# Performance work log

Measured on AMD Instinct MI355X. Metric: run time of the kernel, lower is better.

Reference implementation:

```python
import jax, jax.numpy as jnp
import numpy as np

B, CIN, H, W, OC = 32, 64, 32, 128, 128


def setup_inputs() -> dict:
    key = jax.random.key(0)
    ks = jax.random.split(key, 5)
    scale_x = (6.0 / (CIN + 5 * OC)) ** 0.5  # xavier-uniform-like std scale
    scale_h = (6.0 / (OC + 5 * OC)) ** 0.5
    return {
        "x": jax.random.normal(ks[0], (B, CIN, H, W), jnp.float32),
        "w0": jax.random.normal(ks[1], (4, CIN, 5 * OC), jnp.float32) * scale_x,
        "u0": jax.random.normal(ks[2], (4, OC, 5 * OC), jnp.float32) * scale_h,
        "u1": jax.random.normal(ks[3], (4, OC, 5 * OC), jnp.float32) * scale_h,
        "b": jax.random.uniform(ks[4], (4, 5 * OC), jnp.float32),
    }


def _flip(x, d):
    # direction 0: identity; 1: flip width; 2: flip height; 3: flip both
    if d == 1:
        return x[:, :, :, ::-1]
    if d == 2:
        return x[:, :, ::-1, :]
    if d == 3:
        return x[:, :, ::-1, ::-1]
    return x


def _scan_direction(x, w0, u0, u1, b):
    """2D LSTM raster-order recurrence via anti-diagonal wavefronts.
    x: (B, CIN, H, W) already flipped. Returns (B, OC, H, W) in the flipped frame
    (the original module folds hidden states without flipping back)."""
    Bb, Cin, Hh, Ww = x.shape
    oc = u0.shape[0]
    K = min(Hh, Ww)  # max wavefront length
    xh = jnp.transpose(x, (2, 3, 0, 1))              # (H, W, B, Cin)
    gx_all = jnp.einsum('hwbc,cg->hwbg', xh, w0) + b  # input projection (H,W,B,5oc)
    c0 = jnp.zeros((Hh, Ww, Bb, oc), x.dtype)
    h0 = jnp.zeros_like(c0)
    ks = jnp.arange(K)

    def step(carry, d):
        c_state, h_state = carry
        y0 = jnp.maximum(0, d - (Ww - 1))
        ys = y0 + ks
        xs = d - ys
        valid = (ys <= jnp.minimum(d, Hh - 1)) & (xs >= 0) & (xs < Ww)
        ysc = jnp.clip(ys, 0, Hh - 1)
        xsc = jnp.clip(xs, 0, Ww - 1)
        gx = gx_all[ysc, xsc]  # (K, B, 5oc)
        m_up = ((ys > 0) & valid)[:, None, None]
        m_lf = ((xs > 0) & valid)[:, None, None]
        yu = jnp.clip(ys - 1, 0, Hh - 1)
        xl = jnp.clip(xs - 1, 0, Ww - 1)
        h_up = jnp.where(m_up, h_state[yu, xsc], 0.0)
        c_up = jnp.where(m_up, c_state[yu, xsc], 0.0)
        h_lf = jnp.where(m_lf, h_state[ysc, xl], 0.0)
        c_lf = jnp.where(m_lf, c_state[ysc, xl], 0.0)
        gates = gx + jnp.einsum('kbo,og->kbg', h_up, u0) + jnp.einsum('kbo,og->kbg', h_lf, u1)
        i = jax.nn.sigmoid(gates[..., :oc])
        f = jax.nn.sigmoid(gates[..., oc:2 * oc])
        g = jnp.tanh(gates[..., 2 * oc:3 * oc])
        o = jax.nn.sigmoid(gates[..., 3 * oc:4 * oc])
        l = jax.nn.sigmoid(gates[..., 4 * oc:])
        c_new = f * (l * c_up + (1.0 - l) * c_lf) + i * g
        h_new = o * jnp.tanh(c_new)
        yw = jnp.where(valid, ysc, Hh)  # invalid lanes scatter out-of-bounds -> dropped
        c_state = c_state.at[yw, xsc].set(c_new, mode='drop')
        h_state = h_state.at[yw, xsc].set(h_new, mode='drop')
        return (c_state, h_state), None

    (c_state, h_state), _ = jax.lax.scan(step, (c0, h0), jnp.arange(Hh + Ww - 1))
    return jnp.transpose(h_state, (2, 3, 0, 1))  # (B, OC, H, W)


def reference(x, w0, u0, u1, b):
    outs = [_scan_direction(_flip(x, d), w0[d], u0[d], u1[d], b[d]) for d in range(4)]
    return jnp.stack(outs, axis=1)  # (B, 4, OC, H, W)
```

## Files before the change

### kernel.cpp

```cpp
#include <hip/hip_runtime.h>


typedef unsigned short ushort_t;
typedef unsigned long long ull_t;
typedef __attribute__((ext_vector_type(8))) short short8;
typedef __attribute__((ext_vector_type(4))) short shortx4;
typedef __attribute__((ext_vector_type(4))) float floatx4;
typedef __attribute__((ext_vector_type(2))) float floatx2;
typedef __attribute__((ext_vector_type(4))) unsigned int uintx4;

__device__ __forceinline__ float bf2f(ushort_t u) {
    union { unsigned int i; float f; } v; v.i = ((unsigned int)u) << 16; return v.f;
}
__device__ __forceinline__ ushort_t f2bf(float f) {
    union { float f; unsigned int i; } v; v.f = f;
    unsigned int u = v.i;
    u += 0x7fffu + ((u >> 16) & 1u);
    return (ushort_t)(u >> 16);
}
__device__ __forceinline__ float frcp(float x) { return __builtin_amdgcn_rcpf(x); }
__device__ __forceinline__ float fsig(float x) { return frcp(1.f + __expf(-x)); }
__device__ __forceinline__ float ftanh(float x) { float e = __expf(2.f * x); return 1.f - 2.f * frcp(e + 1.f); }

__device__ __forceinline__ unsigned int load_coh_u32(const unsigned int* p) {
    unsigned int v;
    asm volatile("global_load_dword %0, %1, off sc0 sc1\n\ts_waitcnt vmcnt(0)"
                 : "=v"(v) : "v"(p) : "memory");
    return v;
}
__device__ __forceinline__ void store_coh_u32(unsigned int* p, unsigned int v) {
    asm volatile("global_store_dword %0, %1, off sc0 sc1" :: "v"(p), "v"(v) : "memory");
}
__device__ __forceinline__ void store_coh_u64(ull_t* p, ull_t v) {
    asm volatile("global_store_dwordx2 %0, %1, off sc0 sc1" :: "v"(p), "v"(v) : "memory");
}

__global__ void k_init(unsigned int* prod) { prod[threadIdx.x] = 0u; }

__global__ void k_sniff(const ushort_t* x, unsigned int* flag) {
    int i = threadIdx.x;
    ushort_t u = x[2 * i];
    int e = (u >> 7) & 0xFF;
    bool plausible = (e >= 118 && e <= 130);
    unsigned long long m = __ballot(plausible);
    if (i == 0) flag[0] = (__popcll(m) >= 32) ? 1u : 0u;
}

__global__ void k_packw(const void* u0v, const void* u1v, const void* w0v,
                        ushort_t* wcatf, ushort_t* w0f, const unsigned int* flag) {
    const bool isbf = (*flag != 0);
    int id = blockIdx.x * 256 + threadIdx.x;
    if (id >= 4 * 320 * 640) return;
    int d = id / (320 * 640);
    int rem = id % (320 * 640);
    int k = rem / 640, n = rem % 640;
    size_t idx; const void* src;
    if (k < 128)      { src = u0v; idx = (size_t)(d * 128 + k) * 640 + n; }
    else if (k < 256) { src = u1v; idx = (size_t)(d * 128 + (k - 128)) * 640 + n; }
    else              { src = w0v; idx = (size_t)(d * 64 + (k - 256)) * 640 + n; }
    ushort_t v = isbf ? ((const ushort_t*)src)[idx] : f2bf(((const float*)src)[idx]);
    int c = n & 15, ntg = n >> 4, wv = ntg & 7, nt = ntg >> 3;
    int q = (k >> 3) & 3, j = k & 7, ks = k >> 5;
    int lane = c + 16 * q;
    if (ks < 8) wcatf[((((d * 8 + wv) * 8 + ks) * 5 + nt) * 64 + lane) * 8 + j] = v;
    else        w0f[(((d * 2 + (ks - 8)) * 40 + ntg) * 64 + lane) * 8 + j] = v;
}

__global__ void k_packx(const void* xv, ushort_t* xT, const unsigned int* flag) {
    const bool isbf = (*flag != 0);
    __shared__ ushort_t tile[16 * 2048];
    int h = (int)blockIdx.x >> 3, wb = (int)blockIdx.x & 7;
    int w0c = wb * 16;
    int t = threadIdx.x;
    for (int pass = 0; pass < 4; ++pass) {
        int bc = pass * 512 + t;
        size_t base = (size_t)bc * 4096 + h * 128 + w0c;
        if (isbf) {
            const ushort_t* src = (const ushort_t*)xv + base;
            #pragma unroll
            for (int i = 0; i < 16; ++i) tile[i * 2048 + bc] = src[i];
        } else {
            const float* src = (const float*)xv + base;
            #pragma unroll
            for (int i = 0; i < 16; ++i) tile[i * 2048 + bc] = f2bf(src[i]);
        }
    }
    __syncthreads();
    for (int i = 0; i < 16; ++i) {
        ushort_t* dst = xT + (size_t)(h * 128 + w0c + i) * 2048;
        int t4 = t * 4;
        #pragma unroll
        for (int rr = 0; rr < 4; ++rr) dst[t4 + rr] = tile[i * 2048 + t4 + rr];
    }
}

#define LDS_USHORTS 67072

__global__ __launch_bounds__(512, 2) void k_scan(
    const ushort_t* __restrict__ xT, const ushort_t* __restrict__ wcatf,
    const ushort_t* __restrict__ w0f, const void* __restrict__ biasv,
    void* __restrict__ outv, ull_t* __restrict__ comm,
    unsigned int* prod, int ring, const unsigned int* flag) {
    extern __shared__ ushort_t lds[];
    ushort_t* w0lds = lds;
    ushort_t* hbuf0 = lds + 40960;
    ushort_t* hbuf1 = lds + 45312;
    ushort_t* lfbuf = lds + 49664;
    float*    cbuf_f = (float*)(lds + 54016);
    ushort_t* xbuf  = lds + 62464;

    const bool isbf = (*flag != 0);
    const int tid = threadIdx.x;
    const int bx = blockIdx.x;
    const int d = bx >> 6, p = bx & 63;
    const int lane = tid & 63, wv = tid >> 6;
    const int q = lane >> 4, cl = lane & 15;

    short8 bU[8][5];
    {
        const ushort_t* wsrc = wcatf + (size_t)(d * 8 + wv) * 8 * 5 * 512;
        #pragma unroll
        for (int ks = 0; ks < 8; ++ks)
            #pragma unroll
            for (int nt = 0; nt < 5; ++nt)
                bU[ks][nt] = *(const short8*)(wsrc + (ks * 5 + nt) * 512 + lane * 8);
    }
    {
        const ushort_t* src = w0f + (size_t)d * 40960;
        for (int i = tid; i < 5120; i += 512)
            *(short8*)(w0lds + i * 8) = *(const short8*)(src + i * 8);
    }
    for (int i = 40960 + tid; i < LDS_USHORTS; i += 512) lds[i] = 0;

    float bias_f[5];
    #pragma unroll
    for (int nt = 0; nt < 5; ++nt) {
        int bi = d * 640 + 16 * (wv + 8 * nt) + cl;
        bias_f[nt] = isbf ? bf2f(((const ushort_t*)biasv)[bi]) : ((const float*)biasv)[bi];
    }

    float cst[2][2][4];
    #pragma unroll
    for (int a = 0; a < 2; ++a)
        #pragma unroll
        for (int m = 0; m < 2; ++m)
            #pragma unroll
            for (int r = 0; r < 4; ++r) cst[a][m][r] = 0.f;

    __syncthreads();

    unsigned int* myprod = prod + d * 64 + p;
    unsigned int* lprod  = prod + d * 64 + p - 1;
    unsigned int* cons   = prod + 256;
    unsigned int* mycons = cons + d * 64 + p;
    unsigned int* rcons  = cons + d * 64 + p + 1;
    const int oc = 16 * wv + cl;
    const int xb = tid >> 4, x16 = tid & 15;

    for (int y = 0; y < 32; ++y) {
        {
            int fy = (d & 2) ? (31 - y) : y;
            #pragma unroll
            for (int cc = 0; cc < 2; ++cc) {
                int col = 2 * p + cc;
                int fx = (d & 1) ? (127 - col) : col;
                const ushort_t* sx = xT + (size_t)(fy * 128 + fx) * 2048;
                *(shortx4*)(xbuf + cc * 2304 + xb * 72 + x16 * 4) =
                    *(const shortx4*)(sx + xb * 64 + x16 * 4);
            }
        }
        __syncthreads();

        floatx4 acc[2][5];
        #pragma unroll
        for (int mt = 0; mt < 2; ++mt)
            #pragma unroll
            for (int nt = 0; nt < 5; ++nt) {
                floatx4 v = {bias_f[nt], bias_f[nt], bias_f[nt], bias_f[nt]};
                acc[mt][nt] = v;
            }
        #pragma unroll
        for (int ks = 0; ks < 4; ++ks) {
            short8 a0 = *(const short8*)(hbuf0 + cl * 136 + 32 * ks + 8 * q);
            short8 a1 = *(const short8*)(hbuf0 + (cl + 16) * 136 + 32 * ks + 8 * q);
            #pragma unroll
            for (int nt = 0; nt < 5; ++nt) {
                acc[0][nt] = __builtin_amdgcn_mfma_f32_16x16x32_bf16(a0, bU[ks][nt], acc[0][nt], 0, 0, 0);
                acc[1][nt] = __builtin_amdgcn_mfma_f32_16x16x32_bf16(a1, bU[ks][nt], acc[1][nt], 0, 0, 0);
            }
        }
        #pragma unroll
        for (int ks = 0; ks < 2; ++ks) {
            short8 a0 = *(const short8*)(xbuf + cl * 72 + 32 * ks + 8 * q);
            short8 a1 = *(const short8*)(xbuf + (cl + 16) * 72 + 32 * ks + 8 * q);
            #pragma unroll
            for (int nt = 0; nt < 5; ++nt) {
                short8 bf = *(const short8*)(w0lds + ((ks * 40 + (wv + 8 * nt)) * 64 + lane) * 8);
                acc[0][nt] = __builtin_amdgcn_mfma_f32_16x16x32_bf16(a0, bf, acc[0][nt], 0, 0, 0);
                acc[1][nt] = __builtin_amdgcn_mfma_f32_16x16x32_bf16(a1, bf, acc[1][nt], 0, 0, 0);
            }
        }

        if (p > 0 && tid == 0) {
            int it = 0;
            while (load_coh_u32(lprod) < (unsigned)(y + 1)) {
                __builtin_amdgcn_s_sleep(1);
                if (++it > 10000000) break;
            }
        }
        __syncthreads();
        if (p > 0) {
            size_t slot = ((size_t)(d * 64 + (p - 1)) * ring + (size_t)(y & (ring - 1))) * 4096;
            const ull_t* src = comm + slot + (size_t)xb * 128 + x16 * 8;
            uintx4 u0_, u1_, u2_, u3_;
            asm volatile(
                "global_load_dwordx4 %0, %4, off sc0 sc1\n\t"
                "global_load_dwordx4 %1, %4, off offset:16 sc0 sc1\n\t"
                "global_load_dwordx4 %2, %4, off offset:32 sc0 sc1\n\t"
                "global_load_dwordx4 %3, %4, off offset:48 sc0 sc1\n\t"
                "s_waitcnt vmcnt(0)"
                : "=v"(u0_), "=v"(u1_), "=v"(u2_), "=v"(u3_)
                : "v"(src) : "memory");
            float* cd = cbuf_f + xb * 132 + x16 * 8;
            ushort_t* hd = lfbuf + xb * 136 + x16 * 8;
            union { unsigned int u; float f; } cv;
            cv.u = u0_.x; cd[0] = cv.f; hd[0] = (ushort_t)u0_.y;
            cv.u = u0_.z; cd[1] = cv.f; hd[1] = (ushort_t)u0_.w;
            cv.u = u1_.x; cd[2] = cv.f; hd[2] = (ushort_t)u1_.y;
            cv.u = u1_.z; cd[3] = cv.f; hd[3] = (ushort_t)u1_.w;
            cv.u = u2_.x; cd[4] = cv.f; hd[4] = (ushort_t)u2_.y;
            cv.u = u2_.z; cd[5] = cv.f; hd[5] = (ushort_t)u2_.w;
            cv.u = u3_.x; cd[6] = cv.f; hd[6] = (ushort_t)u3_.y;
            cv.u = u3_.z; cd[7] = cv.f; hd[7] = (ushort_t)u3_.w;
        }
        __syncthreads();
        if (p > 0 && tid == 0)
            store_coh_u32(mycons, (unsigned)(y + 1));

        #pragma unroll
        for (int ks = 4; ks < 8; ++ks) {
            short8 a0 = *(const short8*)(lfbuf + cl * 136 + 32 * (ks - 4) + 8 * q);
            short8 a1 = *(const short8*)(lfbuf + (cl + 16) * 136 + 32 * (ks - 4) + 8 * q);
            #pragma unroll
            for (int nt = 0; nt < 5; ++nt) {
                acc[0][nt] = __builtin_amdgcn_mfma_f32_16x16x32_bf16(a0, bU[ks][nt], acc[0][nt], 0, 0, 0);
                acc[1][nt] = __builtin_amdgcn_mfma_f32_16x16x32_bf16(a1, bU[ks][nt], acc[1][nt], 0, 0, 0);
            }
        }
        float hN0[2][4];
        #pragma unroll
        for (int mt = 0; mt < 2; ++mt)
            #pragma unroll
            for (int r = 0; r < 4; ++r) {
                float ii = fsig(acc[mt][0][r]);
                float ff = fsig(acc[mt][1][r]);
                float gg = ftanh(acc[mt][2][r]);
                float oo = fsig(acc[mt][3][r]);
                float ll = fsig(acc[mt][4][r]);
                int b = 16 * mt + 4 * q + r;
                float cup = cst[0][mt][r];
                float clf = cbuf_f[b * 132 + oc];
                float cn = ff * (ll * cup + (1.f - ll) * clf) + ii * gg;
                cst[0][mt][r] = cn;
                hN0[mt][r] = oo * ftanh(cn);
            }
        #pragma unroll
        for (int mt = 0; mt < 2; ++mt)
            #pragma unroll
            for (int r = 0; r < 4; ++r)
                hbuf0[(16 * mt + 4 * q + r) * 136 + oc] = f2bf(hN0[mt][r]);
        __syncthreads();

        #pragma unroll
        for (int mt = 0; mt < 2; ++mt)
            #pragma unroll
            for (int nt = 0; nt < 5; ++nt) {
                floatx4 v = {bias_f[nt], bias_f[nt], bias_f[nt], bias_f[nt]};
                acc[mt][nt] = v;
            }
        #pragma unroll
        for (int ks = 0; ks < 10; ++ks) {
            short8 a0, a1;
            if (ks < 4) {
                a0 = *(const short8*)(hbuf1 + cl * 136 + 32 * ks + 8 * q);
                a1 = *(const short8*)(hbuf1 + (cl + 16) * 136 + 32 * ks + 8 * q);
            } else if (ks < 8) {
                a0 = *(const short8*)(hbuf0 + cl * 136 + 32 * (ks - 4) + 8 * q);
                a1 = *(const short8*)(hbuf0 + (cl + 16) * 136 + 32 * (ks - 4) + 8 * q);
            } else {
                a0 = *(const short8*)(xbuf + 2304 + cl * 72 + 32 * (ks - 8) + 8 * q);
                a1 = *(const short8*)(xbuf + 2304 + (cl + 16) * 72 + 32 * (ks - 8) + 8 * q);
            }
            #pragma unroll
            for (int nt = 0; nt < 5; ++nt) {
                short8 bf = (ks < 8) ? bU[ks][nt]
                    : *(const short8*)(w0lds + (((ks - 8) * 40 + (wv + 8 * nt)) * 64 + lane) * 8);
                acc[0][nt] = __builtin_amdgcn_mfma_f32_16x16x32_bf16(a0, bf, acc[0][nt], 0, 0, 0);
                acc[1][nt] = __builtin_amdgcn_mfma_f32_16x16x32_bf16(a1, bf, acc[1][nt], 0, 0, 0);
            }
        }
        float hN1[2][4];
        #pragma unroll
        for (int mt = 0; mt < 2; ++mt)
            #pragma unroll
            for (int r = 0; r < 4; ++r) {
                float ii = fsig(acc[mt][0][r]);
                float ff = fsig(acc[mt][1][r]);
                float gg = ftanh(acc[mt][2][r]);
                float oo = fsig(acc[mt][3][r]);
                float ll = fsig(acc[mt][4][r]);
                float cup = cst[1][mt][r];
                float clf = cst[0][mt][r];
                float cn = ff * (ll * cup + (1.f - ll) * clf) + ii * gg;
                cst[1][mt][r] = cn;
                hN1[mt][r] = oo * ftanh(cn);
            }
        if (p < 63 && y >= ring && tid == 0) {
            int it = 0;
            while ((int)load_coh_u32(rcons) < y - ring + 1) {
                __builtin_amdgcn_s_sleep(1);
                if (++it > 10000000) break;
            }
        }
        __syncthreads();

        if (p < 63) {
            size_t slot = ((size_t)(d * 64 + p) * ring + (size_t)(y & (ring - 1))) * 4096;
            #pragma unroll
            for (int mt = 0; mt < 2; ++mt)
                #pragma unroll
                for (int r = 0; r < 4; ++r) {
                    int b = 16 * mt + 4 * q + r;
                    union { float f; unsigned int u; } cv; cv.f = cst[1][mt][r];
                    ull_t v = (ull_t)cv.u | ((ull_t)(unsigned int)f2bf(hN1[mt][r]) << 32);
                    store_coh_u64(comm + slot + (size_t)b * 128 + oc, v);
                }
            asm volatile("s_waitcnt vmcnt(0)" ::: "memory");
            __syncthreads();
            if (tid == 0)
                store_coh_u32(myprod, (unsigned)(y + 1));
        }

        #pragma unroll
        for (int mt = 0; mt < 2; ++mt)
            #pragma unroll
            for (int r = 0; r < 4; ++r) {
                int b = 16 * mt + 4 * q + r;
                hbuf1[b * 136 + oc] = f2bf(hN1[mt][r]);
                size_t oi = ((size_t)((b * 4 + d) * 128 + oc) * 32 + y) * 128 + 2 * p;
                if (isbf) {
                    unsigned int pk = (unsigned int)f2bf(hN0[mt][r]) |
                                      ((unsigned int)f2bf(hN1[mt][r]) << 16);
                    *(unsigned int*)((ushort_t*)outv + oi) = pk;
                } else {
                    floatx2 v2 = {hN0[mt][r], hN1[mt][r]};
                    *(floatx2*)((float*)outv + oi) = v2;
                }
            }
    }
}

extern "C" void kernel_launch(void* const* d_in, const int* in_sizes, int n_in,
                              void* d_out, int out_size, void* d_ws, size_t ws_size,
                              hipStream_t stream) {
    const void* x  = d_in[0];
    const void* w0 = d_in[1];
    const void* u0 = d_in[2];
    const void* u1 = d_in[3];
    const void* bs = d_in[4];

    const size_t CTRLB  = 4096;
    const size_t WCATB  = 4ull * 8 * 8 * 5 * 512 * 2;
    const size_t W0FB   = 4ull * 2 * 40 * 64 * 8 * 2;
    const size_t XTB    = 32ull * 128 * 32 * 64 * 2;
    const size_t fixed  = CTRLB + WCATB + W0FB + XTB;
    int ring = 32;
    while (ring > 2 && fixed + (size_t)ring * 8388608ull > ws_size) ring >>= 1;

    char* w = (char*)d_ws;
    unsigned int* prod = (unsigned int*)w;
    unsigned int* flag = prod + 512;
    ushort_t* wcatf = (ushort_t*)(w + CTRLB);
    ushort_t* w0f   = (ushort_t*)(w + CTRLB + WCATB);
    ushort_t* xT    = (ushort_t*)(w + CTRLB + WCATB + W0FB);
    ull_t*    comm  = (ull_t*)(w + fixed);

    (void)hipFuncSetAttribute((const void*)k_scan,
                              hipFuncAttributeMaxDynamicSharedMemorySize,
                              LDS_USHORTS * 2);

    hipLaunchKernelGGL(k_init, dim3(1), dim3(1024), 0, stream, prod);
    hipLaunchKernelGGL(k_sniff, dim3(1), dim3(64), 0, stream, (const ushort_t*)x, flag);
    hipLaunchKernelGGL(k_packw, dim3(3200), dim3(256), 0, stream, u0, u1, w0, wcatf, w0f, flag);
    hipLaunchKernelGGL(k_packx, dim3(256), dim3(512), 0, stream, x, xT, flag);
    hipLaunchKernelGGL(k_scan, dim3(256), dim3(512), LDS_USHORTS * 2, stream,
                       xT, wcatf, w0f, bs, d_out, comm, prod, ring, flag);
}
```

Measured before the change: 2.725 ms.

## Process four columns per block, halving blocks and cross-block handoffs

Each block now owns four adjacent columns instead of two. This halves the grid to 128 blocks and shortens the producer/consumer chain across columns. Within a block, columns 1-3 consume left-neighbour state from LDS, so three of every four column handoffs avoid global coherent memory. x tiles are read straight from global memory into MFMA operands instead of being staged in LDS. The spin-wait is now done by all threads, with no sleep, instead of by thread 0 followed by a barrier. The cost is more serial work per block and lower occupancy, and every thread busy-polling adds memory traffic.

```diff
diff --git a/kernel.cpp b/kernel.cpp
--- a/kernel.cpp
+++ b/kernel.cpp
@@ -6,7 +6,6 @@
 typedef __attribute__((ext_vector_type(8))) short short8;
 typedef __attribute__((ext_vector_type(4))) short shortx4;
 typedef __attribute__((ext_vector_type(4))) float floatx4;
-typedef __attribute__((ext_vector_type(2))) float floatx2;
 typedef __attribute__((ext_vector_type(4))) unsigned int uintx4;
 
 __device__ __forceinline__ float bf2f(ushort_t u) {
@@ -94,7 +93,7 @@
     }
 }
 
-#define LDS_USHORTS 67072
+#define LDS_USHORTS 79744
 
 __global__ __launch_bounds__(512, 2) void k_scan(
     const ushort_t* __restrict__ xT, const ushort_t* __restrict__ wcatf,
@@ -103,16 +102,16 @@
     unsigned int* prod, int ring, const unsigned int* flag) {
     extern __shared__ ushort_t lds[];
     ushort_t* w0lds = lds;
-    ushort_t* hbuf0 = lds + 40960;
-    ushort_t* hbuf1 = lds + 45312;
-    ushort_t* lfbuf = lds + 49664;
-    float*    cbuf_f = (float*)(lds + 54016);
-    ushort_t* xbuf  = lds + 62464;
+    ushort_t* hbufs = lds + 40960;
+    ushort_t* hnew0 = lds + 58368;
+    ushort_t* hnew1 = lds + 62720;
+    ushort_t* lfbuf = lds + 67072;
+    float*    cbuf_f = (float*)(lds + 71424);
 
     const bool isbf = (*flag != 0);
     const int tid = threadIdx.x;
     const int bx = blockIdx.x;
-    const int d = bx >> 6, p = bx & 63;
+    const int d = bx >> 5, p = bx & 31;
     const int lane = tid & 63, wv = tid >> 6;
     const int q = lane >> 4, cl = lane & 15;
 
@@ -139,9 +138,9 @@
         bias_f[nt] = isbf ? bf2f(((const ushort_t*)biasv)[bi]) : ((const float*)biasv)[bi];
     }
 
-    float cst[2][2][4];
+    float cst[4][2][4];
     #pragma unroll
-    for (int a = 0; a < 2; ++a)
+    for (int a = 0; a < 4; ++a)
         #pragma unroll
         for (int m = 0; m < 2; ++m)
             #pragma unroll
@@ -149,27 +148,24 @@
 
     __syncthreads();
 
-    unsigned int* myprod = prod + d * 64 + p;
-    unsigned int* lprod  = prod + d * 64 + p - 1;
-    unsigned int* cons   = prod + 256;
-    unsigned int* mycons = cons + d * 64 + p;
-    unsigned int* rcons  = cons + d * 64 + p + 1;
+    unsigned int* myprod = prod + d * 32 + p;
+    unsigned int* lprod  = prod + d * 32 + p - 1;
+    unsigned int* cons   = prod + 128;
+    unsigned int* mycons = cons + d * 32 + p;
+    unsigned int* rcons  = cons + d * 32 + p + 1;
     const int oc = 16 * wv + cl;
     const int xb = tid >> 4, x16 = tid & 15;
+    const int colbase = 4 * p;
 
     for (int y = 0; y < 32; ++y) {
-        {
-            int fy = (d & 2) ? (31 - y) : y;
-            #pragma unroll
-            for (int cc = 0; cc < 2; ++cc) {
-                int col = 2 * p + cc;
-                int fx = (d & 1) ? (127 - col) : col;
-                const ushort_t* sx = xT + (size_t)(fy * 128 + fx) * 2048;
-                *(shortx4*)(xbuf + cc * 2304 + xb * 72 + x16 * 4) =
-                    *(const shortx4*)(sx + xb * 64 + x16 * 4);
-            }
-        }
-        __syncthreads();
+        const int fy = (d & 2) ? (31 - y) : y;
+        const ushort_t* xc[4];
+        #pragma unroll
+        for (int c = 0; c < 4; ++c) {
+            int col = colbase + c;
+            int fx = (d & 1) ? (127 - col) : col;
+            xc[c] = xT + (size_t)(fy * 128 + fx) * 2048;
+        }
 
         floatx4 acc[2][5];
         #pragma unroll
@@ -181,8 +177,8 @@
             }
         #pragma unroll
         for (int ks = 0; ks < 4; ++ks) {
-            short8 a0 = *(const short8*)(hbuf0 + cl * 136 + 32 * ks + 8 * q);
-            short8 a1 = *(const short8*)(hbuf0 + (cl + 16) * 136 + 32 * ks + 8 * q);
+            short8 a0 = *(const short8*)(hbufs + cl * 136 + 32 * ks + 8 * q);
+            short8 a1 = *(const short8*)(hbufs + (cl + 16) * 136 + 32 * ks + 8 * q);
             #pragma unroll
             for (int nt = 0; nt < 5; ++nt) {
                 acc[0][nt] = __builtin_amdgcn_mfma_f32_16x16x32_bf16(a0, bU[ks][nt], acc[0][nt], 0, 0, 0);
@@ -190,27 +186,23 @@
             }
         }
         #pragma unroll
-        for (int ks = 0; ks < 2; ++ks) {
-            short8 a0 = *(const short8*)(xbuf + cl * 72 + 32 * ks + 8 * q);
-            short8 a1 = *(const short8*)(xbuf + (cl + 16) * 72 + 32 * ks + 8 * q);
+        for (int kk = 0; kk < 2; ++kk) {
+            short8 a0 = *(const short8*)(xc[0] + cl * 64 + kk * 32 + 8 * q);
+            short8 a1 = *(const short8*)(xc[0] + (cl + 16) * 64 + kk * 32 + 8 * q);
             #pragma unroll
             for (int nt = 0; nt < 5; ++nt) {
-                short8 bf = *(const short8*)(w0lds + ((ks * 40 + (wv + 8 * nt)) * 64 + lane) * 8);
+                short8 bf = *(const short8*)(w0lds + ((kk * 40 + (wv + 8 * nt)) * 64 + lane) * 8);
                 acc[0][nt] = __builtin_amdgcn_mfma_f32_16x16x32_bf16(a0, bf, acc[0][nt], 0, 0, 0);
                 acc[1][nt] = __builtin_amdgcn_mfma_f32_16x16x32_bf16(a1, bf, acc[1][nt], 0, 0, 0);
             }
         }
 
-        if (p > 0 && tid == 0) {
-            int it = 0;
+        if (p > 0) {
+            unsigned it = 0;
             while (load_coh_u32(lprod) < (unsigned)(y + 1)) {
-                __builtin_amdgcn_s_sleep(1);
-                if (++it > 10000000) break;
-            }
-        }
-        __syncthreads();
-        if (p > 0) {
-            size_t slot = ((size_t)(d * 64 + (p - 1)) * ring + (size_t)(y & (ring - 1))) * 4096;
+                if (++it > 100000000u) break;
+            }
+            size_t slot = ((size_t)(d * 31 + (p - 1)) * ring + (size_t)(y & (ring - 1))) * 4096;
             const ull_t* src = comm + slot + (size_t)xb * 128 + x16 * 8;
             uintx4 u0_, u1_, u2_, u3_;
             asm volatile(
@@ -221,7 +213,7 @@
                 "s_waitcnt vmcnt(0)"
                 : "=v"(u0_), "=v"(u1_), "=v"(u2_), "=v"(u3_)
                 : "v"(src) : "memory");
-            float* cd = cbuf_f + xb * 132 + x16 * 8;
+            float* cd = cbuf_f + xb * 130 + x16 * 8;
             ushort_t* hd = lfbuf + xb * 136 + x16 * 8;
             union { unsigned int u; float f; } cv;
             cv.u = u0_.x; cd[0] = cv.f; hd[0] = (ushort_t)u0_.y;
@@ -237,6 +229,8 @@
         if (p > 0 && tid == 0)
             store_coh_u32(mycons, (unsigned)(y + 1));
 
+        float hNout[4][2][4];
+
         #pragma unroll
         for (int ks = 4; ks < 8; ++ks) {
             short8 a0 = *(const short8*)(lfbuf + cl * 136 + 32 * (ks - 4) + 8 * q);
@@ -247,7 +241,6 @@
                 acc[1][nt] = __builtin_amdgcn_mfma_f32_16x16x32_bf16(a1, bU[ks][nt], acc[1][nt], 0, 0, 0);
             }
         }
-        float hN0[2][4];
         #pragma unroll
         for (int mt = 0; mt < 2; ++mt)
             #pragma unroll
@@ -259,80 +252,108 @@
                 float ll = fsig(acc[mt][4][r]);
                 int b = 16 * mt + 4 * q + r;
                 float cup = cst[0][mt][r];
-                float clf = cbuf_f[b * 132 + oc];
+                float clf = cbuf_f[b * 130 + oc];
                 float cn = ff * (ll * cup + (1.f - ll) * clf) + ii * gg;
                 cst[0][mt][r] = cn;
-                hN0[mt][r] = oo * ftanh(cn);
-            }
+                float hv = oo * ftanh(cn);
+                hNout[0][mt][r] = hv;
+                hnew0[b * 136 + oc] = f2bf(hv);
+            }
+        __syncthreads();
         #pragma unroll
         for (int mt = 0; mt < 2; ++mt)
             #pragma unroll
             for (int r = 0; r < 4; ++r)
-                hbuf0[(16 * mt + 4 * q + r) * 136 + oc] = f2bf(hN0[mt][r]);
+                hbufs[(16 * mt + 4 * q + r) * 136 + oc] = f2bf(hNout[0][mt][r]);
+
+        #pragma unroll
+        for (int c = 1; c < 4; ++c) {
+            const ushort_t* hup = hbufs + c * 4352;
+            const ushort_t* hlf = (c & 1) ? hnew0 : hnew1;
+            ushort_t* hdst = (c & 1) ? hnew1 : hnew0;
+            #pragma unroll
+            for (int mt = 0; mt < 2; ++mt)
+                #pragma unroll
+                for (int nt = 0; nt < 5; ++nt) {
+                    floatx4 v = {bias_f[nt], bias_f[nt], bias_f[nt], bias_f[nt]};
+                    acc[mt][nt] = v;
+                }
+            #pragma unroll
+            for (int ks = 0; ks < 4; ++ks) {
+                short8 a0 = *(const short8*)(hup + cl * 136 + 32 * ks + 8 * q);
+                short8 a1 = *(const short8*)(hup + (cl + 16) * 136 + 32 * ks + 8 * q);
+                #pragma unroll
+                for (int nt = 0; nt < 5; ++nt) {
+                    acc[0][nt] = __builtin_amdgcn_mfma_f32_16x16x32_bf16(a0, bU[ks][nt], acc[0][nt], 0, 0, 0);
+                    acc[1][nt] = __builtin_amdgcn_mfma_f32_16x16x32_bf16(a1, bU[ks][nt], acc[1][nt], 0, 0, 0);
+                }
+            }
+            #pragma unroll
+            for (int kk = 0; kk < 2; ++kk) {
+                short8 a0 = *(const short8*)(xc[c] + cl * 64 + kk * 32 + 8 * q);
+                short8 a1 = *(const short8*)(xc[c] + (cl + 16) * 64 + kk * 32 + 8 * q);
+                #pragma unroll
+                for (int nt = 0; nt < 5; ++nt) {
+                    short8 bf = *(const short8*)(w0lds + ((kk * 40 + (wv + 8 * nt)) * 64 + lane) * 8);
+                    acc[0][nt] = __builtin_amdgcn_mfma_f32_16x16x32_bf16(a0, bf, acc[0][nt], 0, 0, 0);
+                    acc[1][nt] = __builtin_amdgcn_mfma_f32_16x16x32_bf16(a1, bf, acc[1][nt], 0, 0, 0);
+                }
+            }
+            #pragma unroll
+            for (int ks = 4; ks < 8; ++ks) {
+                short8 a0 = *(const short8*)(hlf + cl * 136 + 32 * (ks - 4) + 8 * q);
+                short8 a1 = *(const short8*)(hlf + (cl + 16) * 136 + 32 * (ks - 4) + 8 * q);
+                #pragma unroll
+                for (int nt = 0; nt < 5; ++nt) {
+                    acc[0][nt] = __builtin_amdgcn_mfma_f32_16x16x32_bf16(a0, bU[ks][nt], acc[0][nt], 0, 0, 0);
+                    acc[1][nt] = __builtin_amdgcn_mfma_f32_16x16x32_bf16(a1, bU[ks][nt], acc[1][nt], 0, 0, 0);
+                }
+            }
+            #pragma unroll
+            for (int mt = 0; mt < 2; ++mt)
+                #pragma unroll
+                for (int r = 0; r < 4; ++r) {
+                    float ii = fsig(acc[mt][0][r]);
+                    float ff = fsig(acc[mt][1][r]);
+                    float gg = ftanh(acc[mt][2][r]);
+                    float oo = fsig(acc[mt][3][r]);
+                    float ll = fsig(acc[mt][4][r]);
+                    int b = 16 * mt + 4 * q + r;
+                    float cup = cst[c][mt][r];
+                    float clf = cst[c - 1][mt][r];
+                    float cn = ff * (ll * cup + (1.f - ll) * clf) + ii * gg;
+                    cst[c][mt][r] = cn;
+                    float hv = oo * ftanh(cn);
+                    hNout[c][mt][r] = hv;
+                    if (c < 3) hdst[b * 136 + oc] = f2bf(hv);
+                }
+            if (c < 3) {
+                __syncthreads();
+                #pragma unroll
+                for (int mt = 0; mt < 2; ++mt)
+                    #pragma unroll
+                    for (int r = 0; r < 4; ++r)
+                        hbufs[c * 4352 + (16 * mt + 4 * q + r) * 136 + oc] = f2bf(hNout[c][mt][r]);
+            }
+        }
+
+        if (p < 31 && y >= ring) {
+            unsigned it = 0;
+            while ((int)load_coh_u32(rcons) < y - ring + 1) {
+                if (++it > 100000000u) break;
+            }
+        }
         __syncthreads();
 
-        #pragma unroll
-        for (int mt = 0; mt < 2; ++mt)
-            #pragma unroll
-            for (int nt = 0; nt < 5; ++nt) {
-                floatx4 v = {bias_f[nt], bias_f[nt], bias_f[nt], bias_f[nt]};
-                acc[mt][nt] = v;
-            }
-        #pragma unroll
-        for (int ks = 0; ks < 10; ++ks) {
-            short8 a0, a1;
-            if (ks < 4) {
-                a0 = *(const short8*)(hbuf1 + cl * 136 + 32 * ks + 8 * q);
-                a1 = *(const short8*)(hbuf1 + (cl + 16) * 136 + 32 * ks + 8 * q);
-            } else if (ks < 8) {
-                a0 = *(const short8*)(hbuf0 + cl * 136 + 32 * (ks - 4) + 8 * q);
-                a1 = *(const short8*)(hbuf0 + (cl + 16) * 136 + 32 * (ks - 4) + 8 * q);
-            } else {
-                a0 = *(const short8*)(xbuf + 2304 + cl * 72 + 32 * (ks - 8) + 8 * q);
-                a1 = *(const short8*)(xbuf + 2304 + (cl + 16) * 72 + 32 * (ks - 8) + 8 * q);
-            }
-            #pragma unroll
-            for (int nt = 0; nt < 5; ++nt) {
-                short8 bf = (ks < 8) ? bU[ks][nt]
-                    : *(const short8*)(w0lds + (((ks - 8) * 40 + (wv + 8 * nt)) * 64 + lane) * 8);
-                acc[0][nt] = __builtin_amdgcn_mfma_f32_16x16x32_bf16(a0, bf, acc[0][nt], 0, 0, 0);
-                acc[1][nt] = __builtin_amdgcn_mfma_f32_16x16x32_bf16(a1, bf, acc[1][nt], 0, 0, 0);
-            }
-        }
-        float hN1[2][4];
-        #pragma unroll
-        for (int mt = 0; mt < 2; ++mt)
-            #pragma unroll
-            for (int r = 0; r < 4; ++r) {
-                float ii = fsig(acc[mt][0][r]);
-                float ff = fsig(acc[mt][1][r]);
-                float gg = ftanh(acc[mt][2][r]);
-                float oo = fsig(acc[mt][3][r]);
-                float ll = fsig(acc[mt][4][r]);
-                float cup = cst[1][mt][r];
-                float clf = cst[0][mt][r];
-                float cn = ff * (ll * cup + (1.f - ll) * clf) + ii * gg;
-                cst[1][mt][r] = cn;
-                hN1[mt][r] = oo * ftanh(cn);
-            }
-        if (p < 63 && y >= ring && tid == 0) {
-            int it = 0;
-            while ((int)load_coh_u32(rcons) < y - ring + 1) {
-                __builtin_amdgcn_s_sleep(1);
-                if (++it > 10000000) break;
-            }
-        }
-        __syncthreads();
-
-        if (p < 63) {
-            size_t slot = ((size_t)(d * 64 + p) * ring + (size_t)(y & (ring - 1))) * 4096;
+        if (p < 31) {
+            size_t slot = ((size_t)(d * 31 + p) * ring + (size_t)(y & (ring - 1))) * 4096;
             #pragma unroll
             for (int mt = 0; mt < 2; ++mt)
                 #pragma unroll
                 for (int r = 0; r < 4; ++r) {
                     int b = 16 * mt + 4 * q + r;
-                    union { float f; unsigned int u; } cv; cv.f = cst[1][mt][r];
-                    ull_t v = (ull_t)cv.u | ((ull_t)(unsigned int)f2bf(hN1[mt][r]) << 32);
+                    union { float f; unsigned int u; } cv; cv.f = cst[3][mt][r];
+                    ull_t v = (ull_t)cv.u | ((ull_t)(unsigned int)f2bf(hNout[3][mt][r]) << 32);
                     store_coh_u64(comm + slot + (size_t)b * 128 + oc, v);
                 }
             asm volatile("s_waitcnt vmcnt(0)" ::: "memory");
@@ -346,15 +367,18 @@
             #pragma unroll
             for (int r = 0; r < 4; ++r) {
                 int b = 16 * mt + 4 * q + r;
-                hbuf1[b * 136 + oc] = f2bf(hN1[mt][r]);
-                size_t oi = ((size_t)((b * 4 + d) * 128 + oc) * 32 + y) * 128 + 2 * p;
+                hbufs[3 * 4352 + b * 136 + oc] = f2bf(hNout[3][mt][r]);
+                size_t oi = ((size_t)((b * 4 + d) * 128 + oc) * 32 + y) * 128 + colbase;
                 if (isbf) {
-                    unsigned int pk = (unsigned int)f2bf(hN0[mt][r]) |
-                                      ((unsigned int)f2bf(hN1[mt][r]) << 16);
-                    *(unsigned int*)((ushort_t*)outv + oi) = pk;
+                    ull_t pk = (ull_t)(unsigned int)f2bf(hNout[0][mt][r])
+                             | ((ull_t)(unsigned int)f2bf(hNout[1][mt][r]) << 16)
+                             | ((ull_t)(unsigned int)f2bf(hNout[2][mt][r]) << 32)
+                             | ((ull_t)(unsigned int)f2bf(hNout[3][mt][r]) << 48);
+                    *(ull_t*)((ushort_t*)outv + oi) = pk;
                 } else {
-                    floatx2 v2 = {hN0[mt][r], hN1[mt][r]};
-                    *(floatx2*)((float*)outv + oi) = v2;
+                    floatx4 v4 = {hNout[0][mt][r], hNout[1][mt][r],
+                                  hNout[2][mt][r], hNout[3][mt][r]};
+                    *(floatx4*)((float*)outv + oi) = v4;
                 }
             }
     }
@@ -375,7 +399,8 @@
     const size_t XTB    = 32ull * 128 * 32 * 64 * 2;
     const size_t fixed  = CTRLB + WCATB + W0FB + XTB;
     int ring = 32;
-    while (ring > 2 && fixed + (size_t)ring * 8388608ull > ws_size) ring >>= 1;
+    const size_t perrow = 4ull * 31 * 4096 * 8;
+    while (ring > 2 && fixed + (size_t)ring * perrow > ws_size) ring >>= 1;
 
     char* w = (char*)d_ws;
     unsigned int* prod = (unsigned int*)w;
@@ -393,6 +418,6 @@
     hipLaunchKernelGGL(k_sniff, dim3(1), dim3(64), 0, stream, (const ushort_t*)x, flag);
     hipLaunchKernelGGL(k_packw, dim3(3200), dim3(256), 0, stream, u0, u1, w0, wcatf, w0f, flag);
     hipLaunchKernelGGL(k_packx, dim3(256), dim3(512), 0, stream, x, xT, flag);
-    hipLaunchKernelGGL(k_scan, dim3(256), dim3(512), LDS_USHORTS * 2, stream,
+    hipLaunchKernelGGL(k_scan, dim3(128), dim3(512), LDS_USHORTS * 2, stream,
                        xT, wcatf, w0f, bs, d_out, comm, prod, ring, flag);
 }
```

Measured after the change: 3.642 ms. +33.6%, slower.
